# Kernel optimization log

Hardware: AMD Instinct MI355X
Metric: run time of the kernel (lower is better)

Reference implementation:

```python
import jax, jax.numpy as jnp
import numpy as np

B, NIN, NOUT, CIN, COUT = 32, 512, 128, 128, 32
NUM_ITERS = 10


def setup_inputs() -> dict:
    key = jax.random.key(0)
    k1, k2, k3 = jax.random.split(key, 3)
    x = jax.random.normal(k1, (B, NIN, CIN), dtype=jnp.float32)
    y = jax.random.randint(k2, (B,), 0, NOUT)  # unused by forward, kept for signature fidelity
    # xavier_uniform over W1 [1,Nin,Nout,Cout,Cin] (torch fan_in=Nin*Nout*Cout... use gain-1 approx on last two dims)
    limit = float(np.sqrt(6.0 / (CIN + COUT)))
    W1 = jax.random.uniform(k3, (NIN, NOUT, COUT, CIN), dtype=jnp.float32, minval=-limit, maxval=limit)
    return {"x": x, "W1": W1, "y": y}


def _forward(x, W1):
    # u_hat[b,n,m,o] = sum_c W1[n,m,o,c] * x[b,n,c]   -- per-(in,out) capsule linear transform
    u_hat = jnp.einsum('nmoc,bnc->bnmo', W1, x)  # [B, Nin, Nout, Cout]
    b0 = jnp.zeros(u_hat.shape[:3], dtype=u_hat.dtype)  # [B, Nin, Nout]

    def step(b, _):
        c = jax.nn.softmax(b, axis=2)                        # route weights over output capsules
        s = jnp.einsum('bnm,bnmo->bmo', c, u_hat)            # weighted sum over input capsules
        # squash_v1 with axis=1 on a singleton dim in the original -> elementwise degenerate form
        s2 = s * s
        v = (jnp.sqrt(s2) / (0.5 + s2)) * s                  # [B, Nout, Cout]
        agree = jnp.einsum('bmo,bnmo->bnm', v, u_hat)        # agreement update
        return b + agree, v

    _, vs = jax.lax.scan(step, b0, None, length=NUM_ITERS)
    poses = vs[-1]                                            # [B, Nout, Cout]
    activations = jnp.sqrt(jnp.sum(poses * poses, axis=2))    # [B, Nout]
    return poses, activations


def reference(x, W1, y):
    return _forward(x, W1)
```

## Files before the change

kernel.cpp:

```cpp
#include <hip/hip_runtime.h>
#include <hip/hip_bf16.h>
#include <stdint.h>
#include <math.h>

#define NIN_  512
#define NOUT_ 128
#define CIN_  128
#define COUT_ 32
#define MO_   4096
#define NQ_   64

typedef __attribute__((ext_vector_type(4))) float f32x4;

__global__ __launch_bounds__(256) void k_build(const float* __restrict__ x,
                                               const float* __restrict__ W1,
                                               float* __restrict__ u,
                                               int NB, int b0) {
    const int n   = blockIdx.x >> 4;
    const int mt  = blockIdx.x & 15;
    const int mo0 = mt * 256;
    const int t   = threadIdx.x;
    const int l   = t & 63;
    const int bg  = t >> 6;

    __shared__ f32x4 xs4[32 * 32];
    __shared__ f32x4 ws4[256 * 8];

    const int nxu = NB * 32;
    for (int k = t; k < nxu; k += 256) {
        const int bl = k >> 5;
        const int cu = k & 31;
        xs4[k] = *(const f32x4*)(x + (((size_t)(b0 + bl) * NIN_ + n) * CIN_ + cu * 4));
    }

    const int cu8 = t & 7;
    const int row = t >> 3;
    const int active = (bg < (NB >> 3));

    float acc[4][8];
#pragma unroll
    for (int i = 0; i < 4; ++i)
#pragma unroll
        for (int j = 0; j < 8; ++j) acc[i][j] = 0.f;

    f32x4 wr[8];
#pragma unroll
    for (int p = 0; p < 8; ++p) {
        const int ml = row + p * 32;
        wr[p] = *(const f32x4*)(W1 + ((size_t)(n * MO_ + mo0 + ml) * CIN_ + 0 * 32 + cu8 * 4));
    }

    for (int ch = 0; ch < 4; ++ch) {
        __syncthreads();
#pragma unroll
        for (int p = 0; p < 8; ++p) {
            const int ml = row + p * 32;
            ws4[ml * 8 + (cu8 ^ (ml & 7))] = wr[p];
        }
        __syncthreads();
        if (ch < 3) {
#pragma unroll
            for (int p = 0; p < 8; ++p) {
                const int ml = row + p * 32;
                wr[p] = *(const f32x4*)(W1 + ((size_t)(n * MO_ + mo0 + ml) * CIN_ + (ch + 1) * 32 + cu8 * 4));
            }
        }
        if (active) {
#pragma unroll
            for (int c4 = 0; c4 < 8; ++c4) {
                f32x4 wv[4];
#pragma unroll
                for (int i = 0; i < 4; ++i)
                    wv[i] = ws4[(l + i * 64) * 8 + (c4 ^ (l & 7))];
                f32x4 xq[8];
#pragma unroll
                for (int j = 0; j < 8; ++j)
                    xq[j] = xs4[(bg * 8 + j) * 32 + ch * 8 + c4];
#pragma unroll
                for (int i = 0; i < 4; ++i)
#pragma unroll
                    for (int j = 0; j < 8; ++j) {
                        acc[i][j] += wv[i][0] * xq[j][0];
                        acc[i][j] += wv[i][1] * xq[j][1];
                        acc[i][j] += wv[i][2] * xq[j][2];
                        acc[i][j] += wv[i][3] * xq[j][3];
                    }
            }
        }
    }

    if (active) {
#pragma unroll
        for (int i = 0; i < 4; ++i)
#pragma unroll
            for (int j = 0; j < 8; ++j)
                u[((size_t)n * NB + bg * 8 + j) * MO_ + mo0 + i * 64 + l] = acc[i][j];
    }
}

template<int MODE>
__global__ __launch_bounds__(256) void k_route(const float* __restrict__ u,
                                               const float* __restrict__ vws,
                                               float* __restrict__ blog,
                                               float* __restrict__ spart,
                                               int NB) {
    const int nbg = NB >> 2;
    const int bg  = blockIdx.x % nbg;
    const int q   = blockIdx.x / nbg;
    const int w   = threadIdx.x >> 6;
    const int l   = threadIdx.x & 63;
    const int bl  = bg * 4 + w;
    const int sub = l >> 3;

    f32x4 vr[16];
    if (MODE != 0) {
#pragma unroll
        for (int j = 0; j < 16; ++j)
            vr[j] = *(const f32x4*)(vws + (size_t)bl * MO_ + (j * 64 + l) * 4);
    }

    f32x4 sacc[16];
#pragma unroll
    for (int j = 0; j < 16; ++j) sacc[j] = (f32x4){0.f, 0.f, 0.f, 0.f};

    for (int nn = 0; nn < 8; ++nn) {
        const int n = q * 8 + nn;
        const f32x4* up = (const f32x4*)(u + ((size_t)n * NB + bl) * MO_);
        f32x4 ur[16];
#pragma unroll
        for (int j = 0; j < 16; ++j) ur[j] = up[j * 64 + l];

        if (MODE == 0) {
            const float cu = 1.0f / 128.0f;
#pragma unroll
            for (int j = 0; j < 16; ++j) {
                sacc[j][0] += cu * ur[j][0]; sacc[j][1] += cu * ur[j][1];
                sacc[j][2] += cu * ur[j][2]; sacc[j][3] += cu * ur[j][3];
            }
        } else {
            float* bp = blog + ((size_t)bl * NIN_ + n) * NOUT_;
            float bn[16];
            float mx = -1e30f;
#pragma unroll
            for (int j = 0; j < 16; ++j) {
                float p = vr[j][0] * ur[j][0] + vr[j][1] * ur[j][1]
                        + vr[j][2] * ur[j][2] + vr[j][3] * ur[j][3];
                p += __shfl_xor(p, 1, 64);
                p += __shfl_xor(p, 2, 64);
                p += __shfl_xor(p, 4, 64);
                const float old = (MODE == 1) ? 0.f : bp[j * 8 + sub];
                bn[j] = old + p;
                mx = fmaxf(mx, bn[j]);
            }
            if ((l & 7) == 0) {
#pragma unroll
                for (int j = 0; j < 16; ++j) bp[j * 8 + sub] = bn[j];
            }
            mx = fmaxf(mx, __shfl_xor(mx, 8, 64));
            mx = fmaxf(mx, __shfl_xor(mx, 16, 64));
            mx = fmaxf(mx, __shfl_xor(mx, 32, 64));
            float se = 0.f;
#pragma unroll
            for (int j = 0; j < 16; ++j) {
                bn[j] = expf(bn[j] - mx);
                se += bn[j];
            }
            se += __shfl_xor(se, 8, 64);
            se += __shfl_xor(se, 16, 64);
            se += __shfl_xor(se, 32, 64);
            const float inv = 1.0f / se;
#pragma unroll
            for (int j = 0; j < 16; ++j) {
                const float c = bn[j] * inv;
                sacc[j][0] += c * ur[j][0]; sacc[j][1] += c * ur[j][1];
                sacc[j][2] += c * ur[j][2]; sacc[j][3] += c * ur[j][3];
            }
        }
    }

    f32x4* sp = (f32x4*)(spart + ((size_t)q * NB + bl) * MO_);
#pragma unroll
    for (int j = 0; j < 16; ++j) sp[j * 64 + l] = sacc[j];
}

__global__ __launch_bounds__(256) void k_squash_mid(const float* __restrict__ spart,
                                                    float* __restrict__ vws, int NB) {
    const int j = blockIdx.x * 256 + threadIdx.x;
    const size_t stride = (size_t)NB * MO_;
    float s = 0.f;
#pragma unroll
    for (int q = 0; q < NQ_; ++q) s += spart[q * stride + j];
    const float s2 = s * s;
    vws[j] = (sqrtf(s2) / (0.5f + s2)) * s;
}

__global__ __launch_bounds__(256) void k_squash_fin(const float* __restrict__ spart,
                                                    float* __restrict__ out,
                                                    int NB, int b0) {
    const int j = blockIdx.x * 256 + threadIdx.x;
    const size_t stride = (size_t)NB * MO_;
    float s = 0.f;
#pragma unroll
    for (int q = 0; q < NQ_; ++q) s += spart[q * stride + j];
    const float s2 = s * s;
    const float v = (sqrtf(s2) / (0.5f + s2)) * s;
    out[(size_t)b0 * MO_ + j] = v;

    float v2 = v * v;
#pragma unroll
    for (int d = 16; d >= 1; d >>= 1) v2 += __shfl_xor(v2, d, 64);
    if ((j & 31) == 0) {
        const int bl = j >> 12;
        const int m  = (j >> 5) & 127;
        out[131072 + (size_t)(b0 + bl) * NOUT_ + m] = sqrtf(v2);
    }
}

extern "C" void kernel_launch(void* const* d_in, const int* in_sizes, int n_in,
                              void* d_out, int out_size, void* d_ws, size_t ws_size,
                              hipStream_t stream) {
    const float* x  = (const float*)d_in[0];
    const float* W1 = (const float*)d_in[1];
    float* out = (float*)d_out;

    const size_t need32 = (size_t)32 * NIN_ * MO_ * 4
                        + (size_t)32 * NIN_ * NOUT_ * 4
                        + (size_t)32 * MO_ * 4
                        + (size_t)NQ_ * 32 * MO_ * 4;
    const int NB = (ws_size >= need32) ? 32 : 16;
    const int npass = 32 / NB;

    char* ws = (char*)d_ws;
    const size_t bytes_u  = (size_t)NB * NIN_ * MO_ * 4;
    const size_t bytes_bl = (size_t)NB * NIN_ * NOUT_ * 4;
    const size_t bytes_v  = (size_t)NB * MO_ * 4;
    float* u     = (float*)(ws);
    float* blog  = (float*)(ws + bytes_u);
    float* vws   = (float*)(ws + bytes_u + bytes_bl);
    float* spart = (float*)(ws + bytes_u + bytes_bl + bytes_v);

    const int rgrid = (NB / 4) * NQ_;

    for (int pass = 0; pass < npass; ++pass) {
        const int b0 = pass * NB;

        k_build<<<8192, 256, 0, stream>>>(x, W1, u, NB, b0);

        k_route<0><<<rgrid, 256, 0, stream>>>(u, vws, blog, spart, NB);
        k_squash_mid<<<NB * 16, 256, 0, stream>>>(spart, vws, NB);

        for (int it = 1; it <= 9; ++it) {
            if (it == 1) k_route<1><<<rgrid, 256, 0, stream>>>(u, vws, blog, spart, NB);
            else         k_route<2><<<rgrid, 256, 0, stream>>>(u, vws, blog, spart, NB);
            if (it < 9) k_squash_mid<<<NB * 16, 256, 0, stream>>>(spart, vws, NB);
            else        k_squash_fin<<<NB * 16, 256, 0, stream>>>(spart, out, NB, b0);
        }
    }
}
```

Before: 1.136 ms.

## Split routing work across two waves per batch and vectorize squash reduction

Each routing block now covers a single batch with two 64-lane waves. Each wave owns half of the output-capsule chunks and holds only 8 u vectors in registers instead of 16. To keep the softmax exact, each wave also recomputes the agreement logits for the other half, so the u and v loads for the logit step are duplicated. The blog buffer is ping-ponged so one wave can write while both read, and squash_mid is vectorized with f32x4 loads. The aim is lower register pressure and higher occupancy in the memory-bound route kernel, paid for with extra u traffic and double the blog workspace.

```diff
diff --git a/kernel.cpp b/kernel.cpp
--- a/kernel.cpp
+++ b/kernel.cpp
@@ -98,100 +98,145 @@
     }
 }
 
-template<int MODE>
-__global__ __launch_bounds__(256) void k_route(const float* __restrict__ u,
-                                               const float* __restrict__ vws,
-                                               float* __restrict__ blog,
-                                               float* __restrict__ spart,
-                                               int NB) {
-    const int nbg = NB >> 2;
-    const int bg  = blockIdx.x % nbg;
-    const int q   = blockIdx.x / nbg;
-    const int w   = threadIdx.x >> 6;
-    const int l   = threadIdx.x & 63;
-    const int bl  = bg * 4 + w;
+template<int MODE, int H>
+static __device__ __forceinline__ void route_chunk(const float* __restrict__ u,
+                                                   const float* __restrict__ vws,
+                                                   const float* __restrict__ blogR,
+                                                   float* __restrict__ blogW,
+                                                   float* __restrict__ spart,
+                                                   int NB, int bl, int q, int l) {
     const int sub = l >> 3;
 
-    f32x4 vr[16];
-    if (MODE != 0) {
-#pragma unroll
-        for (int j = 0; j < 16; ++j)
-            vr[j] = *(const f32x4*)(vws + (size_t)bl * MO_ + (j * 64 + l) * 4);
-    }
-
-    f32x4 sacc[16];
-#pragma unroll
-    for (int j = 0; j < 16; ++j) sacc[j] = (f32x4){0.f, 0.f, 0.f, 0.f};
+    f32x4 sacc[8];
+#pragma unroll
+    for (int jj = 0; jj < 8; ++jj) sacc[jj] = (f32x4){0.f, 0.f, 0.f, 0.f};
 
     for (int nn = 0; nn < 8; ++nn) {
         const int n = q * 8 + nn;
         const f32x4* up = (const f32x4*)(u + ((size_t)n * NB + bl) * MO_);
-        f32x4 ur[16];
-#pragma unroll
-        for (int j = 0; j < 16; ++j) ur[j] = up[j * 64 + l];
 
         if (MODE == 0) {
             const float cu = 1.0f / 128.0f;
 #pragma unroll
-            for (int j = 0; j < 16; ++j) {
-                sacc[j][0] += cu * ur[j][0]; sacc[j][1] += cu * ur[j][1];
-                sacc[j][2] += cu * ur[j][2]; sacc[j][3] += cu * ur[j][3];
+            for (int jj = 0; jj < 8; ++jj) {
+                const f32x4 uo = up[(H * 8 + jj) * 64 + l];
+                sacc[jj][0] += cu * uo[0]; sacc[jj][1] += cu * uo[1];
+                sacc[jj][2] += cu * uo[2]; sacc[jj][3] += cu * uo[3];
             }
         } else {
-            float* bp = blog + ((size_t)bl * NIN_ + n) * NOUT_;
-            float bn[16];
-            float mx = -1e30f;
-#pragma unroll
-            for (int j = 0; j < 16; ++j) {
-                float p = vr[j][0] * ur[j][0] + vr[j][1] * ur[j][1]
-                        + vr[j][2] * ur[j][2] + vr[j][3] * ur[j][3];
+            const f32x4* vp = (const f32x4*)(vws + (size_t)bl * MO_);
+            const float* bpR = blogR + ((size_t)bl * NIN_ + n) * NOUT_;
+
+            float bnO[8];
+            float bnH[8];
+            f32x4 urh[8];
+            constexpr int OWN = H * 8;
+            constexpr int OTH = 8 - H * 8;
+
+#pragma unroll
+            for (int jj = 0; jj < 8; ++jj) {
+                const int j = OTH + jj;
+                const f32x4 uo = up[j * 64 + l];
+                const f32x4 vo = vp[j * 64 + l];
+                float p = uo[0] * vo[0] + uo[1] * vo[1] + uo[2] * vo[2] + uo[3] * vo[3];
                 p += __shfl_xor(p, 1, 64);
                 p += __shfl_xor(p, 2, 64);
                 p += __shfl_xor(p, 4, 64);
-                const float old = (MODE == 1) ? 0.f : bp[j * 8 + sub];
-                bn[j] = old + p;
-                mx = fmaxf(mx, bn[j]);
-            }
-            if ((l & 7) == 0) {
-#pragma unroll
-                for (int j = 0; j < 16; ++j) bp[j * 8 + sub] = bn[j];
-            }
+                bnO[jj] = ((MODE == 1) ? 0.f : bpR[j * 8 + sub]) + p;
+            }
+#pragma unroll
+            for (int jj = 0; jj < 8; ++jj) {
+                const int j = OWN + jj;
+                urh[jj] = up[j * 64 + l];
+                const f32x4 vo = vp[j * 64 + l];
+                float p = urh[jj][0] * vo[0] + urh[jj][1] * vo[1]
+                        + urh[jj][2] * vo[2] + urh[jj][3] * vo[3];
+                p += __shfl_xor(p, 1, 64);
+                p += __shfl_xor(p, 2, 64);
+                p += __shfl_xor(p, 4, 64);
+                bnH[jj] = ((MODE == 1) ? 0.f : bpR[j * 8 + sub]) + p;
+            }
+
+            if (H == 0 && (l & 7) == 0) {
+                float* bpW = blogW + ((size_t)bl * NIN_ + n) * NOUT_;
+#pragma unroll
+                for (int jj = 0; jj < 8; ++jj) bpW[(OWN + jj) * 8 + sub] = bnH[jj];
+#pragma unroll
+                for (int jj = 0; jj < 8; ++jj) bpW[(OTH + jj) * 8 + sub] = bnO[jj];
+            }
+
+            float mx = -1e30f;
+#pragma unroll
+            for (int jj = 0; jj < 8; ++jj) mx = fmaxf(mx, fmaxf(bnO[jj], bnH[jj]));
             mx = fmaxf(mx, __shfl_xor(mx, 8, 64));
             mx = fmaxf(mx, __shfl_xor(mx, 16, 64));
             mx = fmaxf(mx, __shfl_xor(mx, 32, 64));
-            float se = 0.f;
-#pragma unroll
-            for (int j = 0; j < 16; ++j) {
-                bn[j] = expf(bn[j] - mx);
-                se += bn[j];
-            }
+
+#pragma unroll
+            for (int jj = 0; jj < 8; ++jj) bnO[jj] = expf(bnO[jj] - mx);
+#pragma unroll
+            for (int jj = 0; jj < 8; ++jj) bnH[jj] = expf(bnH[jj] - mx);
+            float seLo = 0.f, seHi = 0.f;
+#pragma unroll
+            for (int jj = 0; jj < 8; ++jj) {
+                if (H == 0) { seLo += bnH[jj]; } else { seLo += bnO[jj]; }
+            }
+#pragma unroll
+            for (int jj = 0; jj < 8; ++jj) {
+                if (H == 0) { seHi += bnO[jj]; } else { seHi += bnH[jj]; }
+            }
+            float se = seLo + seHi;
             se += __shfl_xor(se, 8, 64);
             se += __shfl_xor(se, 16, 64);
             se += __shfl_xor(se, 32, 64);
             const float inv = 1.0f / se;
-#pragma unroll
-            for (int j = 0; j < 16; ++j) {
-                const float c = bn[j] * inv;
-                sacc[j][0] += c * ur[j][0]; sacc[j][1] += c * ur[j][1];
-                sacc[j][2] += c * ur[j][2]; sacc[j][3] += c * ur[j][3];
+
+#pragma unroll
+            for (int jj = 0; jj < 8; ++jj) {
+                const float c = bnH[jj] * inv;
+                sacc[jj][0] += c * urh[jj][0]; sacc[jj][1] += c * urh[jj][1];
+                sacc[jj][2] += c * urh[jj][2]; sacc[jj][3] += c * urh[jj][3];
             }
         }
     }
 
     f32x4* sp = (f32x4*)(spart + ((size_t)q * NB + bl) * MO_);
 #pragma unroll
-    for (int j = 0; j < 16; ++j) sp[j * 64 + l] = sacc[j];
+    for (int jj = 0; jj < 8; ++jj) sp[(H * 8 + jj) * 64 + l] = sacc[jj];
+}
+
+template<int MODE>
+__global__ __launch_bounds__(128, 4) void k_route(const float* __restrict__ u,
+                                                  const float* __restrict__ vws,
+                                                  const float* __restrict__ blogR,
+                                                  float* __restrict__ blogW,
+                                                  float* __restrict__ spart,
+                                                  int NB) {
+    const int bl = blockIdx.x % NB;
+    const int q  = blockIdx.x / NB;
+    const int l  = threadIdx.x & 63;
+    if (threadIdx.x < 64) route_chunk<MODE, 0>(u, vws, blogR, blogW, spart, NB, bl, q, l);
+    else                  route_chunk<MODE, 1>(u, vws, blogR, blogW, spart, NB, bl, q, l);
 }
 
 __global__ __launch_bounds__(256) void k_squash_mid(const float* __restrict__ spart,
                                                     float* __restrict__ vws, int NB) {
-    const int j = blockIdx.x * 256 + threadIdx.x;
-    const size_t stride = (size_t)NB * MO_;
-    float s = 0.f;
-#pragma unroll
-    for (int q = 0; q < NQ_; ++q) s += spart[q * stride + j];
-    const float s2 = s * s;
-    vws[j] = (sqrtf(s2) / (0.5f + s2)) * s;
+    const int j4 = blockIdx.x * 256 + threadIdx.x;
+    const size_t stride4 = (size_t)NB * MO_ / 4;
+    const f32x4* sp4 = (const f32x4*)spart;
+    f32x4 s = {0.f, 0.f, 0.f, 0.f};
+#pragma unroll 8
+    for (int qq = 0; qq < NQ_; ++qq) {
+        const f32x4 v = sp4[(size_t)qq * stride4 + j4];
+        s[0] += v[0]; s[1] += v[1]; s[2] += v[2]; s[3] += v[3];
+    }
+    f32x4 r;
+#pragma unroll
+    for (int c = 0; c < 4; ++c) {
+        const float s2 = s[c] * s[c];
+        r[c] = (sqrtf(s2) / (0.5f + s2)) * s[c];
+    }
+    ((f32x4*)vws)[j4] = r;
 }
 
 __global__ __launch_bounds__(256) void k_squash_fin(const float* __restrict__ spart,
@@ -200,7 +245,7 @@
     const int j = blockIdx.x * 256 + threadIdx.x;
     const size_t stride = (size_t)NB * MO_;
     float s = 0.f;
-#pragma unroll
+#pragma unroll 8
     for (int q = 0; q < NQ_; ++q) s += spart[q * stride + j];
     const float s2 = s * s;
     const float v = (sqrtf(s2) / (0.5f + s2)) * s;
@@ -224,7 +269,7 @@
     float* out = (float*)d_out;
 
     const size_t need32 = (size_t)32 * NIN_ * MO_ * 4
-                        + (size_t)32 * NIN_ * NOUT_ * 4
+                        + (size_t)2 * 32 * NIN_ * NOUT_ * 4
                         + (size_t)32 * MO_ * 4
                         + (size_t)NQ_ * 32 * MO_ * 4;
     const int NB = (ws_size >= need32) ? 32 : 16;
@@ -235,25 +280,30 @@
     const size_t bytes_bl = (size_t)NB * NIN_ * NOUT_ * 4;
     const size_t bytes_v  = (size_t)NB * MO_ * 4;
     float* u     = (float*)(ws);
-    float* blog  = (float*)(ws + bytes_u);
-    float* vws   = (float*)(ws + bytes_u + bytes_bl);
-    float* spart = (float*)(ws + bytes_u + bytes_bl + bytes_v);
-
-    const int rgrid = (NB / 4) * NQ_;
+    float* blogA = (float*)(ws + bytes_u);
+    float* blogB = (float*)(ws + bytes_u + bytes_bl);
+    float* vws   = (float*)(ws + bytes_u + 2 * bytes_bl);
+    float* spart = (float*)(ws + bytes_u + 2 * bytes_bl + bytes_v);
+
+    const int rgrid = NB * NQ_;
+    const int mgrid = (NB * MO_ / 4) / 256;
+    const int fgrid = NB * 16;
 
     for (int pass = 0; pass < npass; ++pass) {
         const int b0 = pass * NB;
 
         k_build<<<8192, 256, 0, stream>>>(x, W1, u, NB, b0);
 
-        k_route<0><<<rgrid, 256, 0, stream>>>(u, vws, blog, spart, NB);
-        k_squash_mid<<<NB * 16, 256, 0, stream>>>(spart, vws, NB);
+        k_route<0><<<rgrid, 128, 0, stream>>>(u, vws, blogA, blogB, spart, NB);
+        k_squash_mid<<<mgrid, 256, 0, stream>>>(spart, vws, NB);
 
         for (int it = 1; it <= 9; ++it) {
-            if (it == 1) k_route<1><<<rgrid, 256, 0, stream>>>(u, vws, blog, spart, NB);
-            else         k_route<2><<<rgrid, 256, 0, stream>>>(u, vws, blog, spart, NB);
-            if (it < 9) k_squash_mid<<<NB * 16, 256, 0, stream>>>(spart, vws, NB);
-            else        k_squash_fin<<<NB * 16, 256, 0, stream>>>(spart, out, NB, b0);
-        }
-    }
-}
+            float* br = (it & 1) ? blogA : blogB;
+            float* bw = (it & 1) ? blogB : blogA;
+            if (it == 1) k_route<1><<<rgrid, 128, 0, stream>>>(u, vws, br, bw, spart, NB);
+            else         k_route<2><<<rgrid, 128, 0, stream>>>(u, vws, br, bw, spart, NB);
+            if (it < 9) k_squash_mid<<<mgrid, 256, 0, stream>>>(spart, vws, NB);
+            else        k_squash_fin<<<fgrid, 256, 0, stream>>>(spart, out, NB, b0);
+        }
+    }
+}
```

Measured after the change: 2.145 ms. 88.7% more time.

## Build u once for all batches and route in two 16-batch halves

Applied to the files above, without the earlier changes.

Computes u_hat for all 32 batches in a single build pass, then runs the routing iterations separately on two halves of 16 batches. Each routing kernel now processes 4 input capsules per block instead of 8, with 128 partial slices. The intent is a smaller per-half working set (u slice, logits, partial sums) that may stay resident in cache across iterations, plus more routing blocks for parallelism. The cost is double the number of routing launches and a longer partial-sum reduction in squash. The code also drops the fallback path and returns without computing anything if the workspace is too small.

```diff
diff --git a/kernel.cpp b/kernel.cpp
--- a/kernel.cpp
+++ b/kernel.cpp
@@ -8,14 +8,16 @@
 #define CIN_  128
 #define COUT_ 32
 #define MO_   4096
-#define NQ_   64
+#define NBT_  32
+#define RB_   16
+#define NPER_ 4
+#define NQP_  128
 
 typedef __attribute__((ext_vector_type(4))) float f32x4;
 
 __global__ __launch_bounds__(256) void k_build(const float* __restrict__ x,
                                                const float* __restrict__ W1,
-                                               float* __restrict__ u,
-                                               int NB, int b0) {
+                                               float* __restrict__ u) {
     const int n   = blockIdx.x >> 4;
     const int mt  = blockIdx.x & 15;
     const int mo0 = mt * 256;
@@ -26,16 +28,14 @@
     __shared__ f32x4 xs4[32 * 32];
     __shared__ f32x4 ws4[256 * 8];
 
-    const int nxu = NB * 32;
-    for (int k = t; k < nxu; k += 256) {
+    for (int k = t; k < NBT_ * 32; k += 256) {
         const int bl = k >> 5;
         const int cu = k & 31;
-        xs4[k] = *(const f32x4*)(x + (((size_t)(b0 + bl) * NIN_ + n) * CIN_ + cu * 4));
+        xs4[k] = *(const f32x4*)(x + (((size_t)bl * NIN_ + n) * CIN_ + cu * 4));
     }
 
     const int cu8 = t & 7;
     const int row = t >> 3;
-    const int active = (bg < (NB >> 3));
 
     float acc[4][8];
 #pragma unroll
@@ -65,37 +65,33 @@
                 wr[p] = *(const f32x4*)(W1 + ((size_t)(n * MO_ + mo0 + ml) * CIN_ + (ch + 1) * 32 + cu8 * 4));
             }
         }
-        if (active) {
-#pragma unroll
-            for (int c4 = 0; c4 < 8; ++c4) {
-                f32x4 wv[4];
-#pragma unroll
-                for (int i = 0; i < 4; ++i)
-                    wv[i] = ws4[(l + i * 64) * 8 + (c4 ^ (l & 7))];
-                f32x4 xq[8];
-#pragma unroll
-                for (int j = 0; j < 8; ++j)
-                    xq[j] = xs4[(bg * 8 + j) * 32 + ch * 8 + c4];
-#pragma unroll
-                for (int i = 0; i < 4; ++i)
-#pragma unroll
-                    for (int j = 0; j < 8; ++j) {
-                        acc[i][j] += wv[i][0] * xq[j][0];
-                        acc[i][j] += wv[i][1] * xq[j][1];
-                        acc[i][j] += wv[i][2] * xq[j][2];
-                        acc[i][j] += wv[i][3] * xq[j][3];
-                    }
-            }
-        }
-    }
-
-    if (active) {
-#pragma unroll
-        for (int i = 0; i < 4; ++i)
+#pragma unroll
+        for (int c4 = 0; c4 < 8; ++c4) {
+            f32x4 wv[4];
+#pragma unroll
+            for (int i = 0; i < 4; ++i)
+                wv[i] = ws4[(l + i * 64) * 8 + (c4 ^ (l & 7))];
+            f32x4 xq[8];
 #pragma unroll
             for (int j = 0; j < 8; ++j)
-                u[((size_t)n * NB + bg * 8 + j) * MO_ + mo0 + i * 64 + l] = acc[i][j];
-    }
+                xq[j] = xs4[(bg * 8 + j) * 32 + ch * 8 + c4];
+#pragma unroll
+            for (int i = 0; i < 4; ++i)
+#pragma unroll
+                for (int j = 0; j < 8; ++j) {
+                    acc[i][j] += wv[i][0] * xq[j][0];
+                    acc[i][j] += wv[i][1] * xq[j][1];
+                    acc[i][j] += wv[i][2] * xq[j][2];
+                    acc[i][j] += wv[i][3] * xq[j][3];
+                }
+        }
+    }
+
+#pragma unroll
+    for (int i = 0; i < 4; ++i)
+#pragma unroll
+        for (int j = 0; j < 8; ++j)
+            u[((size_t)n * NBT_ + bg * 8 + j) * MO_ + mo0 + i * 64 + l] = acc[i][j];
 }
 
 template<int MODE>
@@ -103,10 +99,9 @@
                                                const float* __restrict__ vws,
                                                float* __restrict__ blog,
                                                float* __restrict__ spart,
-                                               int NB) {
-    const int nbg = NB >> 2;
-    const int bg  = blockIdx.x % nbg;
-    const int q   = blockIdx.x / nbg;
+                                               int bofs) {
+    const int bg  = blockIdx.x & 3;
+    const int q   = blockIdx.x >> 2;
     const int w   = threadIdx.x >> 6;
     const int l   = threadIdx.x & 63;
     const int bl  = bg * 4 + w;
@@ -123,9 +118,9 @@
 #pragma unroll
     for (int j = 0; j < 16; ++j) sacc[j] = (f32x4){0.f, 0.f, 0.f, 0.f};
 
-    for (int nn = 0; nn < 8; ++nn) {
-        const int n = q * 8 + nn;
-        const f32x4* up = (const f32x4*)(u + ((size_t)n * NB + bl) * MO_);
+    for (int nn = 0; nn < NPER_; ++nn) {
+        const int n = q * NPER_ + nn;
+        const f32x4* up = (const f32x4*)(u + ((size_t)n * NBT_ + bofs + bl) * MO_);
         f32x4 ur[16];
 #pragma unroll
         for (int j = 0; j < 16; ++j) ur[j] = up[j * 64 + l];
@@ -178,30 +173,30 @@
         }
     }
 
-    f32x4* sp = (f32x4*)(spart + ((size_t)q * NB + bl) * MO_);
+    f32x4* sp = (f32x4*)(spart + ((size_t)q * RB_ + bl) * MO_);
 #pragma unroll
     for (int j = 0; j < 16; ++j) sp[j * 64 + l] = sacc[j];
 }
 
 __global__ __launch_bounds__(256) void k_squash_mid(const float* __restrict__ spart,
-                                                    float* __restrict__ vws, int NB) {
+                                                    float* __restrict__ vws) {
     const int j = blockIdx.x * 256 + threadIdx.x;
-    const size_t stride = (size_t)NB * MO_;
+    const size_t stride = (size_t)RB_ * MO_;
     float s = 0.f;
-#pragma unroll
-    for (int q = 0; q < NQ_; ++q) s += spart[q * stride + j];
+#pragma unroll 8
+    for (int q = 0; q < NQP_; ++q) s += spart[q * stride + j];
     const float s2 = s * s;
     vws[j] = (sqrtf(s2) / (0.5f + s2)) * s;
 }
 
 __global__ __launch_bounds__(256) void k_squash_fin(const float* __restrict__ spart,
                                                     float* __restrict__ out,
-                                                    int NB, int b0) {
+                                                    int b0) {
     const int j = blockIdx.x * 256 + threadIdx.x;
-    const size_t stride = (size_t)NB * MO_;
+    const size_t stride = (size_t)RB_ * MO_;
     float s = 0.f;
-#pragma unroll
-    for (int q = 0; q < NQ_; ++q) s += spart[q * stride + j];
+#pragma unroll 8
+    for (int q = 0; q < NQP_; ++q) s += spart[q * stride + j];
     const float s2 = s * s;
     const float v = (sqrtf(s2) / (0.5f + s2)) * s;
     out[(size_t)b0 * MO_ + j] = v;
@@ -223,37 +218,35 @@
     const float* W1 = (const float*)d_in[1];
     float* out = (float*)d_out;
 
-    const size_t need32 = (size_t)32 * NIN_ * MO_ * 4
-                        + (size_t)32 * NIN_ * NOUT_ * 4
-                        + (size_t)32 * MO_ * 4
-                        + (size_t)NQ_ * 32 * MO_ * 4;
-    const int NB = (ws_size >= need32) ? 32 : 16;
-    const int npass = 32 / NB;
-
     char* ws = (char*)d_ws;
-    const size_t bytes_u  = (size_t)NB * NIN_ * MO_ * 4;
-    const size_t bytes_bl = (size_t)NB * NIN_ * NOUT_ * 4;
-    const size_t bytes_v  = (size_t)NB * MO_ * 4;
+    const size_t bytes_u  = (size_t)NBT_ * NIN_ * MO_ * 4;
+    const size_t bytes_bl = (size_t)RB_ * NIN_ * NOUT_ * 4;
+    const size_t bytes_v  = (size_t)RB_ * MO_ * 4;
+    const size_t bytes_sp = (size_t)NQP_ * RB_ * MO_ * 4;
+    const size_t need = bytes_u + bytes_bl + bytes_v + bytes_sp;
+    if (ws_size < need) return;
+
     float* u     = (float*)(ws);
     float* blog  = (float*)(ws + bytes_u);
     float* vws   = (float*)(ws + bytes_u + bytes_bl);
     float* spart = (float*)(ws + bytes_u + bytes_bl + bytes_v);
 
-    const int rgrid = (NB / 4) * NQ_;
-
-    for (int pass = 0; pass < npass; ++pass) {
-        const int b0 = pass * NB;
-
-        k_build<<<8192, 256, 0, stream>>>(x, W1, u, NB, b0);
-
-        k_route<0><<<rgrid, 256, 0, stream>>>(u, vws, blog, spart, NB);
-        k_squash_mid<<<NB * 16, 256, 0, stream>>>(spart, vws, NB);
+    k_build<<<8192, 256, 0, stream>>>(x, W1, u);
+
+    const int rgrid = (RB_ / 4) * NQP_;
+    const int sgrid = (RB_ * MO_) / 256;
+
+    for (int h = 0; h < 2; ++h) {
+        const int bofs = h * RB_;
+
+        k_route<0><<<rgrid, 256, 0, stream>>>(u, vws, blog, spart, bofs);
+        k_squash_mid<<<sgrid, 256, 0, stream>>>(spart, vws);
 
         for (int it = 1; it <= 9; ++it) {
-            if (it == 1) k_route<1><<<rgrid, 256, 0, stream>>>(u, vws, blog, spart, NB);
-            else         k_route<2><<<rgrid, 256, 0, stream>>>(u, vws, blog, spart, NB);
-            if (it < 9) k_squash_mid<<<NB * 16, 256, 0, stream>>>(spart, vws, NB);
-            else        k_squash_fin<<<NB * 16, 256, 0, stream>>>(spart, out, NB, b0);
-        }
-    }
-}
+            if (it == 1) k_route<1><<<rgrid, 256, 0, stream>>>(u, vws, blog, spart, bofs);
+            else         k_route<2><<<rgrid, 256, 0, stream>>>(u, vws, blog, spart, bofs);
+            if (it < 9) k_squash_mid<<<sgrid, 256, 0, stream>>>(spart, vws);
+            else        k_squash_fin<<<sgrid, 256, 0, stream>>>(spart, out, bofs);
+        }
+    }
+}
```

Measured after the change: 1.036 ms. 1.1x faster.
